# Kernel optimization log

Hardware: AMD Instinct MI355X
Metric: run time of the kernel (lower is better)

The kernel has to match this reference:

```python
import jax, jax.numpy as jnp
import numpy as np

FEATURE_SPACE = 128


def _gru_params(key, in_dim, hidden):
    k1, k2, k3, k4 = jax.random.split(key, 4)
    s = 1.0 / np.sqrt(hidden)
    return (
        jax.random.uniform(k1, (3 * hidden, in_dim), minval=-s, maxval=s, dtype=jnp.float32),
        jax.random.uniform(k2, (3 * hidden, hidden), minval=-s, maxval=s, dtype=jnp.float32),
        jax.random.uniform(k3, (3 * hidden,), minval=-s, maxval=s, dtype=jnp.float32),
        jax.random.uniform(k4, (3 * hidden,), minval=-s, maxval=s, dtype=jnp.float32),
    )


def setup_inputs() -> dict:
    key = jax.random.key(0)
    ks = jax.random.split(key, 6)
    B, T, H, W = 32, 64, 128, 128
    bbox = jax.random.normal(ks[0], (B, T, 4), dtype=jnp.float32)
    flow = jax.random.normal(ks[1], (B, T, H, W, 2), dtype=jnp.float32)
    ego = jax.random.normal(ks[2], (B, T, 3), dtype=jnp.float32)
    Wih_b, Whh_b, bih_b, bhh_b = _gru_params(ks[3], 4, FEATURE_SPACE)
    Wih_f, Whh_f, bih_f, bhh_f = _gru_params(ks[4], 2, FEATURE_SPACE)
    Wih_e, Whh_e, bih_e, bhh_e = _gru_params(ks[5], 3, FEATURE_SPACE)
    return {
        "bbox": bbox, "flow": flow, "ego": ego,
        "Wih_b": Wih_b, "Whh_b": Whh_b, "bih_b": bih_b, "bhh_b": bhh_b,
        "Wih_f": Wih_f, "Whh_f": Whh_f, "bih_f": bih_f, "bhh_f": bhh_f,
        "Wih_e": Wih_e, "Whh_e": Whh_e, "bih_e": bih_e, "bhh_e": bhh_e,
    }


def _gru_encode(x, Wih, Whh, bih, bhh):
    # x: [B, T, D] -> final hidden [B, H], PyTorch GRUCell math, h0 = 0
    B = x.shape[0]
    Hs = Whh.shape[1]
    # precompute input projections for all timesteps: [T, B, 3H]
    gi = jnp.swapaxes(jnp.einsum('btd,gd->btg', x, Wih) + bih, 0, 1)

    def step(h, gi_t):
        gh = h @ Whh.T + bhh
        i_r, i_z, i_n = jnp.split(gi_t, 3, axis=-1)
        h_r, h_z, h_n = jnp.split(gh, 3, axis=-1)
        r = jax.nn.sigmoid(i_r + h_r)
        z = jax.nn.sigmoid(i_z + h_z)
        n = jnp.tanh(i_n + r * h_n)
        h_new = (1.0 - z) * n + z * h
        return h_new, None

    h0 = jnp.zeros((B, Hs), dtype=x.dtype)
    h_final, _ = jax.lax.scan(step, h0, gi)
    return h_final


def reference(bbox, flow, ego,
              Wih_b, Whh_b, bih_b, bhh_b,
              Wih_f, Whh_f, bih_f, bhh_f,
              Wih_e, Whh_e, bih_e, bhh_e):
    mid_x = flow.shape[2] // 2
    mid_y = flow.shape[3] // 2
    # vectorized center-pixel gather: [B, T, 2]
    storage = flow[:, :, mid_x, mid_y, :]
    flow_result = _gru_encode(storage, Wih_f, Whh_f, bih_f, bhh_f)
    bbox_result = _gru_encode(bbox, Wih_b, Whh_b, bih_b, bhh_b)
    ego_result = _gru_encode(ego, Wih_e, Whh_e, bih_e, bhh_e)
    alpha, beta, gamma = 1.0, 1.0, 1.0
    tot = alpha + beta + gamma
    return (flow_result * (beta / tot)
            + bbox_result * (alpha / tot)
            + ego_result * (gamma / tot))
```

## Files before the change

kernel.cpp:

```cpp
#include <hip/hip_runtime.h>
#include <hip/hip_bf16.h>


#define HID 128
#define TT  64
#define BB  32

__global__ __launch_bounds__(384) void gru_fused_kernel(
    const float* __restrict__ bbox, const float* __restrict__ flow, const float* __restrict__ ego,
    const float* __restrict__ Wih_b, const float* __restrict__ Whh_b,
    const float* __restrict__ bih_b, const float* __restrict__ bhh_b,
    const float* __restrict__ Wih_f, const float* __restrict__ Whh_f,
    const float* __restrict__ bih_f, const float* __restrict__ bhh_f,
    const float* __restrict__ Wih_e, const float* __restrict__ Whh_e,
    const float* __restrict__ bih_e, const float* __restrict__ bhh_e,
    float* __restrict__ ws)
{
    const int blk = blockIdx.x;
    const int gru = blk >> 5;
    const int b   = blk & 31;
    const int g   = threadIdx.x;

    const float* Wih; const float* Whh; const float* bih; const float* bhh; int D;
    if (gru == 0)      { Wih = Wih_b; Whh = Whh_b; bih = bih_b; bhh = bhh_b; D = 4; }
    else if (gru == 1) { Wih = Wih_f; Whh = Whh_f; bih = bih_f; bhh = bhh_f; D = 2; }
    else               { Wih = Wih_e; Whh = Whh_e; bih = bih_e; bhh = bhh_e; D = 3; }

    float4 w[32];
    const float4* wrow = reinterpret_cast<const float4*>(Whh + (size_t)g * HID);
    #pragma unroll
    for (int k = 0; k < 32; ++k) w[k] = wrow[k];

    float wih[4] = {0.f, 0.f, 0.f, 0.f};
    for (int d = 0; d < D; ++d) wih[d] = Wih[g * D + d];
    const float bi = bih[g];
    const float bh = bhh[g];

    __shared__ __align__(16) float h_s[HID];
    __shared__ float r_s[HID], z_s[HID], in_s[HID], hn_s[HID];
    __shared__ float x_s[TT][4];

    if (g < TT * 4) {
        const int t = g >> 2, d = g & 3;
        float v = 0.f;
        if (gru == 0) {
            v = bbox[(size_t)(b * TT + t) * 4 + d];
        } else if (gru == 1) {
            if (d < 2) {
                const size_t idx = (((size_t)(b * TT + t) * 128 + 64) * 128 + 64) * 2 + d;
                v = flow[idx];
            }
        } else {
            if (d < 3) v = ego[(size_t)(b * TT + t) * 3 + d];
        }
        x_s[t][d] = v;
    }
    if (g < HID) h_s[g] = 0.f;
    __syncthreads();

    for (int t = 0; t < TT; ++t) {
        float acc = bh;
        #pragma unroll
        for (int k = 0; k < 32; ++k) {
            const float4 hv = reinterpret_cast<const float4*>(h_s)[k];
            acc = fmaf(w[k].x, hv.x, acc);
            acc = fmaf(w[k].y, hv.y, acc);
            acc = fmaf(w[k].z, hv.z, acc);
            acc = fmaf(w[k].w, hv.w, acc);
        }
        float gi = bi;
        #pragma unroll
        for (int d = 0; d < 4; ++d) gi = fmaf(wih[d], x_s[t][d], gi);

        if (g < 256) {
            const float gate = 1.f / (1.f + expf(-(gi + acc)));
            if (g < HID) r_s[g] = gate; else z_s[g - HID] = gate;
        } else {
            in_s[g - 256] = gi;
            hn_s[g - 256] = acc;
        }
        __syncthreads();

        if (g < HID) {
            const float r = r_s[g];
            const float z = z_s[g];
            const float n = tanhf(in_s[g] + r * hn_s[g]);
            h_s[g] = (1.f - z) * n + z * h_s[g];
        }
        __syncthreads();
    }

    if (g < HID) ws[((size_t)gru * BB + b) * HID + g] = h_s[g];
}

__global__ void combine_kernel(const float* __restrict__ ws, float* __restrict__ out) {
    const int i = blockIdx.x * blockDim.x + threadIdx.x;
    if (i < BB * HID) {
        out[i] = (ws[i] + ws[BB * HID + i] + ws[2 * BB * HID + i]) * (1.0f / 3.0f);
    }
}

extern "C" void kernel_launch(void* const* d_in, const int* in_sizes, int n_in,
                              void* d_out, int out_size, void* d_ws, size_t ws_size,
                              hipStream_t stream) {
    const float* bbox  = (const float*)d_in[0];
    const float* flow  = (const float*)d_in[1];
    const float* ego   = (const float*)d_in[2];
    const float* Wih_b = (const float*)d_in[3];
    const float* Whh_b = (const float*)d_in[4];
    const float* bih_b = (const float*)d_in[5];
    const float* bhh_b = (const float*)d_in[6];
    const float* Wih_f = (const float*)d_in[7];
    const float* Whh_f = (const float*)d_in[8];
    const float* bih_f = (const float*)d_in[9];
    const float* bhh_f = (const float*)d_in[10];
    const float* Wih_e = (const float*)d_in[11];
    const float* Whh_e = (const float*)d_in[12];
    const float* bih_e = (const float*)d_in[13];
    const float* bhh_e = (const float*)d_in[14];

    float* ws = (float*)d_ws;
    float* out = (float*)d_out;

    gru_fused_kernel<<<dim3(96), dim3(384), 0, stream>>>(
        bbox, flow, ego,
        Wih_b, Whh_b, bih_b, bhh_b,
        Wih_f, Whh_f, bih_f, bhh_f,
        Wih_e, Whh_e, bih_e, bhh_e,
        ws);

    combine_kernel<<<dim3((BB * HID + 255) / 256), dim3(256), 0, stream>>>(ws, out);
}
```

Baseline: 380.2 us.

## Split GRU hidden units across thread pairs and drop a barrier per step

Each pair of threads now owns one hidden unit and computes all three gate dot products over half of the hidden vector, combining the halves with a lane shuffle. The gate nonlinearities and state update then happen in registers, and the hidden vector is double-buffered in shared memory, so each timestep needs one barrier instead of two and the intermediate gate arrays in shared memory go away. The block shrinks from 384 to 256 threads, which adds redundant input-projection and activation math per pair and 192 weight registers per thread. A dead sigmoid helper is also added.

```diff
diff --git a/kernel.cpp b/kernel.cpp
--- a/kernel.cpp
+++ b/kernel.cpp
@@ -6,7 +6,11 @@
 #define TT  64
 #define BB  32
 
-__global__ __launch_bounds__(384) void gru_fused_kernel(
+__device__ __forceinline__ float sigmoidf_(float x) {
+    return 1.0f / (1.0f + __expf(-x) * 0.0f + expf(-x));
+}
+
+__global__ __launch_bounds__(256, 1) void gru_fused_kernel(
     const float* __restrict__ bbox, const float* __restrict__ flow, const float* __restrict__ ego,
     const float* __restrict__ Wih_b, const float* __restrict__ Whh_b,
     const float* __restrict__ bih_b, const float* __restrict__ bhh_b,
@@ -19,78 +23,95 @@
     const int blk = blockIdx.x;
     const int gru = blk >> 5;
     const int b   = blk & 31;
-    const int g   = threadIdx.x;
+    const int tid = threadIdx.x;
+    const int g   = tid >> 1;
+    const int q   = tid & 1;
 
     const float* Wih; const float* Whh; const float* bih; const float* bhh; int D;
     if (gru == 0)      { Wih = Wih_b; Whh = Whh_b; bih = bih_b; bhh = bhh_b; D = 4; }
     else if (gru == 1) { Wih = Wih_f; Whh = Whh_f; bih = bih_f; bhh = bhh_f; D = 2; }
     else               { Wih = Wih_e; Whh = Whh_e; bih = bih_e; bhh = bhh_e; D = 3; }
 
-    float4 w[32];
-    const float4* wrow = reinterpret_cast<const float4*>(Whh + (size_t)g * HID);
-    #pragma unroll
-    for (int k = 0; k < 32; ++k) w[k] = wrow[k];
+    float4 wr[16], wz[16], wn[16];
+    {
+        const float4* base = reinterpret_cast<const float4*>(Whh) + q * 16;
+        const float4* rowr = base + (size_t)(g        ) * 32;
+        const float4* rowz = base + (size_t)(g + HID  ) * 32;
+        const float4* rown = base + (size_t)(g + 2*HID) * 32;
+        #pragma unroll
+        for (int k = 0; k < 16; ++k) { wr[k] = rowr[k]; wz[k] = rowz[k]; wn[k] = rown[k]; }
+    }
 
-    float wih[4] = {0.f, 0.f, 0.f, 0.f};
-    for (int d = 0; d < D; ++d) wih[d] = Wih[g * D + d];
-    const float bi = bih[g];
-    const float bh = bhh[g];
+    float wir[4] = {0,0,0,0}, wiz[4] = {0,0,0,0}, win[4] = {0,0,0,0};
+    for (int d = 0; d < D; ++d) {
+        wir[d] = Wih[(g        ) * D + d];
+        wiz[d] = Wih[(g + HID  ) * D + d];
+        win[d] = Wih[(g + 2*HID) * D + d];
+    }
+    const float bir = bih[g], biz = bih[g + HID], bin = bih[g + 2*HID];
+    const float bhr = (q == 0) ? bhh[g]         : 0.f;
+    const float bhz = (q == 0) ? bhh[g + HID]   : 0.f;
+    const float bhn = (q == 0) ? bhh[g + 2*HID] : 0.f;
 
-    __shared__ __align__(16) float h_s[HID];
-    __shared__ float r_s[HID], z_s[HID], in_s[HID], hn_s[HID];
-    __shared__ float x_s[TT][4];
+    __shared__ __align__(16) float h_s[2][HID];
+    __shared__ __align__(16) float4 x4_s[TT];
 
-    if (g < TT * 4) {
-        const int t = g >> 2, d = g & 3;
+    {
+        const int t = tid >> 2, d = tid & 3;
         float v = 0.f;
         if (gru == 0) {
             v = bbox[(size_t)(b * TT + t) * 4 + d];
         } else if (gru == 1) {
-            if (d < 2) {
-                const size_t idx = (((size_t)(b * TT + t) * 128 + 64) * 128 + 64) * 2 + d;
-                v = flow[idx];
-            }
+            if (d < 2) v = flow[(((size_t)(b * TT + t) * 128 + 64) * 128 + 64) * 2 + d];
         } else {
             if (d < 3) v = ego[(size_t)(b * TT + t) * 3 + d];
         }
-        x_s[t][d] = v;
+        reinterpret_cast<float*>(&x4_s[t])[d] = v;
     }
-    if (g < HID) h_s[g] = 0.f;
+    if (tid < HID) h_s[0][tid] = 0.f;
+    float h_old = 0.f;
     __syncthreads();
 
+    int cur = 0;
     for (int t = 0; t < TT; ++t) {
-        float acc = bh;
+        const float4 xv = x4_s[t];
+
+        float ar = bhr, az = bhz, an = bhn;
+        const float4* hb = reinterpret_cast<const float4*>(&h_s[cur][q * 64]);
         #pragma unroll
-        for (int k = 0; k < 32; ++k) {
-            const float4 hv = reinterpret_cast<const float4*>(h_s)[k];
-            acc = fmaf(w[k].x, hv.x, acc);
-            acc = fmaf(w[k].y, hv.y, acc);
-            acc = fmaf(w[k].z, hv.z, acc);
-            acc = fmaf(w[k].w, hv.w, acc);
+        for (int k = 0; k < 16; ++k) {
+            const float4 hv = hb[k];
+            ar = fmaf(wr[k].x, hv.x, ar); ar = fmaf(wr[k].y, hv.y, ar);
+            ar = fmaf(wr[k].z, hv.z, ar); ar = fmaf(wr[k].w, hv.w, ar);
+            az = fmaf(wz[k].x, hv.x, az); az = fmaf(wz[k].y, hv.y, az);
+            az = fmaf(wz[k].z, hv.z, az); az = fmaf(wz[k].w, hv.w, az);
+            an = fmaf(wn[k].x, hv.x, an); an = fmaf(wn[k].y, hv.y, an);
+            an = fmaf(wn[k].z, hv.z, an); an = fmaf(wn[k].w, hv.w, an);
         }
-        float gi = bi;
-        #pragma unroll
-        for (int d = 0; d < 4; ++d) gi = fmaf(wih[d], x_s[t][d], gi);
+        ar += __shfl_xor(ar, 1, 64);
+        az += __shfl_xor(az, 1, 64);
+        an += __shfl_xor(an, 1, 64);
 
-        if (g < 256) {
-            const float gate = 1.f / (1.f + expf(-(gi + acc)));
-            if (g < HID) r_s[g] = gate; else z_s[g - HID] = gate;
-        } else {
-            in_s[g - 256] = gi;
-            hn_s[g - 256] = acc;
-        }
+        float gr = bir, gz = biz, gn = bin;
+        gr = fmaf(wir[0], xv.x, gr); gr = fmaf(wir[1], xv.y, gr);
+        gr = fmaf(wir[2], xv.z, gr); gr = fmaf(wir[3], xv.w, gr);
+        gz = fmaf(wiz[0], xv.x, gz); gz = fmaf(wiz[1], xv.y, gz);
+        gz = fmaf(wiz[2], xv.z, gz); gz = fmaf(wiz[3], xv.w, gz);
+        gn = fmaf(win[0], xv.x, gn); gn = fmaf(win[1], xv.y, gn);
+        gn = fmaf(win[2], xv.z, gn); gn = fmaf(win[3], xv.w, gn);
+
+        const float r = 1.f / (1.f + expf(-(gr + ar)));
+        const float z = 1.f / (1.f + expf(-(gz + az)));
+        const float n = tanhf(gn + r * an);
+        const float h_new = (1.f - z) * n + z * h_old;
+        h_old = h_new;
+
+        if (q == 0) h_s[cur ^ 1][g] = h_new;
         __syncthreads();
-
-        if (g < HID) {
-            const float r = r_s[g];
-            const float z = z_s[g];
-            const float n = tanhf(in_s[g] + r * hn_s[g]);
-            h_s[g] = (1.f - z) * n + z * h_s[g];
-        }
-        __syncthreads();
+        cur ^= 1;
     }
 
-    if (g < HID) ws[((size_t)gru * BB + b) * HID + g] = h_s[g];
+    if (q == 0) ws[((size_t)gru * BB + b) * HID + g] = h_old;
 }
 
 __global__ void combine_kernel(const float* __restrict__ ws, float* __restrict__ out) {
@@ -119,10 +140,10 @@
     const float* bih_e = (const float*)d_in[13];
     const float* bhh_e = (const float*)d_in[14];
 
-    float* ws = (float*)d_ws;
+    float* ws  = (float*)d_ws;
     float* out = (float*)d_out;
 
-    gru_fused_kernel<<<dim3(96), dim3(384), 0, stream>>>(
+    gru_fused_kernel<<<dim3(96), dim3(256), 0, stream>>>(
         bbox, flow, ego,
         Wih_b, Whh_b, bih_b, bhh_b,
         Wih_f, Whh_f, bih_f, bhh_f,
```

Result: no change. 374.8 us (-1.4%).
